# Optimization experiments

Measured on AMD Instinct MI355X. Metric: run time of the kernel, lower is better.

Reference implementation:

```python
import jax, jax.numpy as jnp
import numpy as np

# Tsit5 (Tsitouras 2011) explicit RK tableau coefficients (5th-order solution weights)
A21 = 0.161
A31, A32 = -0.008480655492356989, 0.335480655492357
A41, A42, A43 = 2.8971530571054935, -6.359448489975075, 4.3622954328695815
A51, A52, A53, A54 = 5.325864828439257, -11.748883564062828, 7.4955393428898365, -0.09249506636175525
A61, A62, A63, A64, A65 = 5.86145544294642, -12.92096931784711, 8.159367898576159, -0.071584973281401, -0.028269050394068383
B1, B2, B3, B4, B5, B6 = 0.09646076681806523, 0.01, 0.4798896504144996, 1.379008574103742, -3.290069515436081, 2.324710524099774

BATCH, D, H, T = 4096, 64, 256, 128


def net_apply(y, W1, b1, W2, b2):
    # y: [B, D] -> dy/dt: [B, D]  (MLP vector field, autonomous)
    return jnp.tanh(y @ W1 + b1) @ W2 + b2


def tsit5_step(f, y, h):
    # One explicit Tsit5 step of size h on state y: [B, D]
    k1 = f(y)
    k2 = f(y + h * (A21 * k1))
    k3 = f(y + h * (A31 * k1 + A32 * k2))
    k4 = f(y + h * (A41 * k1 + A42 * k2 + A43 * k3))
    k5 = f(y + h * (A51 * k1 + A52 * k2 + A53 * k3 + A54 * k4))
    k6 = f(y + h * (A61 * k1 + A62 * k2 + A63 * k3 + A64 * k4 + A65 * k5))
    return y + h * (B1 * k1 + B2 * k2 + B3 * k3 + B4 * k4 + B5 * k5 + B6 * k6)


def setup_inputs() -> dict:
    key = jax.random.key(0)
    k0, k1, k2 = jax.random.split(key, 3)
    y0 = jax.random.normal(k0, (BATCH, D), dtype=jnp.float32)
    ts = jnp.arange(T, dtype=jnp.float32) * 0.05  # save times
    W1 = jax.random.normal(k1, (D, H), dtype=jnp.float32) / np.sqrt(D)
    b1 = jnp.zeros((H,), dtype=jnp.float32)
    W2 = jax.random.normal(k2, (H, D), dtype=jnp.float32) / np.sqrt(H)
    b2 = jnp.zeros((D,), dtype=jnp.float32)
    return {"y0": y0, "ts": ts, "W1": W1, "b1": b1, "W2": W2, "b2": b2, "n_sub": 8}


def reference(y0, ts, W1, b1, W2, b2, n_sub):
    # Integrate dy/dt = net(y) with fixed-step Tsit5 (n_sub substeps per save interval),
    # returning the trajectory at save points ts: [B, T, D].
    f = lambda y: net_apply(y, W1, b1, W2, b2)

    def interval(y, dt):
        h = dt / n_sub
        def sub(yc, _):
            return tsit5_step(f, yc, h), None
        y, _ = jax.lax.scan(sub, y, None, length=n_sub)
        return y, y

    dts = jnp.diff(ts)                      # [T-1]
    _, ys = jax.lax.scan(interval, y0, dts)  # [T-1, B, D]
    traj = jnp.concatenate([y0[None], ys], axis=0)  # [T, B, D]
    return jnp.transpose(traj, (1, 0, 2))   # [B, T, D]
```

## Files before the change

### kernel.cpp

```cpp
#include <hip/hip_runtime.h>
#include <hip/hip_bf16.h>

typedef __bf16 bf16x8 __attribute__((ext_vector_type(8)));
typedef float f32x4 __attribute__((ext_vector_type(4)));
typedef unsigned int u32;
typedef u32 u32x4 __attribute__((ext_vector_type(4)));

#define MFMA_B16(a,b,c) __builtin_amdgcn_mfma_f32_16x16x32_bf16((a),(b),(c),0,0,0)

#define A21f 0.161f
#define A31f (-0.008480655492356989f)
#define A32f 0.335480655492357f
#define A41f 2.8971530571054935f
#define A42f (-6.359448489975075f)
#define A43f 4.3622954328695815f
#define A51f 5.325864828439257f
#define A52f (-11.748883564062828f)
#define A53f 7.4955393428898365f
#define A54f (-0.09249506636175525f)
#define A61f 5.86145544294642f
#define A62f (-12.92096931784711f)
#define A63f 8.159367898576159f
#define A64f (-0.071584973281401f)
#define A65f (-0.028269050394068383f)
#define B1f 0.09646076681806523f
#define B2f 0.01f
#define B3f 0.4798896504144996f
#define B4f 1.379008574103742f
#define B5f (-3.290069515436081f)
#define B6f 2.324710524099774f

constexpr int T_SAVE = 128;
constexpr int DIM = 64;
constexpr int HID = 256;

__device__ __forceinline__ float fast_exp2(float x){
#if __has_builtin(__builtin_amdgcn_exp2f)
  return __builtin_amdgcn_exp2f(x);
#else
  return exp2f(x);
#endif
}
__device__ __forceinline__ float fast_rcp(float x){
#if __has_builtin(__builtin_amdgcn_rcpf)
  return __builtin_amdgcn_rcpf(x);
#else
  return 1.0f / x;
#endif
}
__device__ __forceinline__ float tanh_fast(float x){
  float t = fast_exp2(x * 2.8853900817779268f);
  return 1.0f - 2.0f * fast_rcp(t + 1.0f);
}
__device__ __forceinline__ f32x4 splat4(float x){ return f32x4{x,x,x,x}; }

__device__ __forceinline__ u32 pack_hl(float x){
  u32 xu = __float_as_uint(x);
  float lo = x - __uint_as_float(xu & 0xFFFF0000u);
  __bf16 lb = (__bf16)lo;
  unsigned short ls; __builtin_memcpy(&ls, &lb, 2);
  return ((u32)ls << 16) | (xu >> 16);
}
__device__ __forceinline__ void unpack2(const u32* p, bf16x8& ah, bf16x8& al){
  union { u32 d[4]; bf16x8 v; } H, L;
#pragma unroll
  for (int j = 0; j < 4; ++j) {
    H.d[j] = __builtin_amdgcn_perm(p[2*j+1], p[2*j], 0x05040100u);
    L.d[j] = __builtin_amdgcn_perm(p[2*j+1], p[2*j], 0x07060302u);
  }
  ah = H.v; al = L.v;
}

__device__ __forceinline__ int bphys(int row, int kq){
  return kq*16 + (row & 8) + ((row & 7) ^ (kq & 7));
}

__global__ __launch_bounds__(512, 2)
void node_tsit5_kernel(const float* __restrict__ y0, const float* __restrict__ ts,
                       const float* __restrict__ W1g, const float* __restrict__ b1g,
                       const float* __restrict__ W2g, const float* __restrict__ b2g,
                       const int* __restrict__ nsub_p, float* __restrict__ out)
{
  const int tid = (int)threadIdx.x;
  const int w   = tid >> 6;
  const int l   = tid & 63;
  const int c   = l & 15;
  const int g   = l >> 4;
  const bool state = (w < 4);
  const int v   = state ? w : (w - 4);
  const int rowbase = (int)blockIdx.x * 16;

  __shared__ __align__(16) u32 Yp[1024];
  __shared__ __align__(16) u32 Hp[4096];
  __shared__ float ts_s[T_SAVE];

  if (tid < T_SAVE) ts_s[tid] = ts[tid];

  const int nsub = nsub_p[0];

  bf16x8 wf[16];
  float bias[4];
  if (state) {
#pragma unroll
    for (int ks = 0; ks < 8; ++ks)
#pragma unroll
      for (int j = 0; j < 8; ++j) {
        float val = W2g[(ks*32 + g*8 + j)*DIM + (v*16 + c)];
        __bf16 hi = (__bf16)val;
        wf[ks*2    ][j] = hi;
        wf[ks*2 + 1][j] = (__bf16)(val - (float)hi);
      }
    bias[0] = b2g[v*16 + c];
    bias[1] = bias[2] = bias[3] = 0.f;
  } else {
#pragma unroll
    for (int t = 0; t < 4; ++t) {
      const int col = (v*4 + t)*16 + c;
#pragma unroll
      for (int sl = 0; sl < 2; ++sl)
#pragma unroll
        for (int j = 0; j < 8; ++j) {
          float val = W1g[(sl*32 + g*8 + j)*HID + col];
          __bf16 hi = (__bf16)val;
          wf[t*4 + sl*2    ][j] = hi;
          wf[t*4 + sl*2 + 1][j] = (__bf16)(val - (float)hi);
        }
      bias[t] = b1g[col];
    }
  }

  const int rdw0 = bphys(c, 2*g    ) * 4;
  const int rdw1 = bphys(c, 2*g + 1) * 4;
  int yw[4];
#pragma unroll
  for (int s = 0; s < 4; ++s) {
    const int kq = (v & 1)*4 + (c >> 2);
    yw[s] = ((v >> 1)*512) + bphys(4*g + s, kq)*4 + (c & 3);
  }
  int hw[4][4];
  if (!state) {
#pragma unroll
    for (int t = 0; t < 4; ++t) {
      const int T = v*4 + t;
      const int kq = (T & 1)*4 + (c >> 2);
#pragma unroll
      for (int r = 0; r < 4; ++r)
        hw[t][r] = ((T >> 1)*512) + bphys(4*g + r, kq)*4 + (c & 3);
    }
  }

  const int d_ = v*16 + c;
  f32x4 y4 = {0.f,0.f,0.f,0.f};
  if (state) {
#pragma unroll
    for (int s = 0; s < 4; ++s) {
      int row = rowbase + 4*g + s;
      y4[s] = y0[row*DIM + d_];
      out[(size_t)row*(T_SAVE*DIM) + d_] = y4[s];
    }
  }
  __syncthreads();

  f32x4 ysv = y4;

  auto feval = [&]() -> f32x4 {
    if (state) {
#pragma unroll
      for (int s = 0; s < 4; ++s) Yp[yw[s]] = pack_hl(ysv[s]);
    }
    __syncthreads();
    if (!state) {
      u32 py[2][8];
      *(u32x4*)&py[0][0] = *(const u32x4*)&Yp[rdw0];
      *(u32x4*)&py[0][4] = *(const u32x4*)&Yp[rdw1];
      *(u32x4*)&py[1][0] = *(const u32x4*)&Yp[512 + rdw0];
      *(u32x4*)&py[1][4] = *(const u32x4*)&Yp[512 + rdw1];
      bf16x8 ah[2], al[2];
      unpack2(py[0], ah[0], al[0]);
      unpack2(py[1], ah[1], al[1]);
#pragma unroll
      for (int t = 0; t < 4; ++t) {
        f32x4 a0 = {0.f,0.f,0.f,0.f}, a1 = {0.f,0.f,0.f,0.f};
        a0 = MFMA_B16(ah[0], wf[t*4 + 0], a0);
        a1 = MFMA_B16(ah[1], wf[t*4 + 2], a1);
        a0 = MFMA_B16(ah[0], wf[t*4 + 1], a0);
        a1 = MFMA_B16(ah[1], wf[t*4 + 3], a1);
        a0 = MFMA_B16(al[0], wf[t*4 + 0], a0);
        a1 = MFMA_B16(al[1], wf[t*4 + 2], a1);
        f32x4 ht = a0 + a1;
#pragma unroll
        for (int r = 0; r < 4; ++r)
          Hp[hw[t][r]] = pack_hl(tanh_fast(ht[r] + bias[t]));
      }
    }
    __syncthreads();
    f32x4 ret = {0.f,0.f,0.f,0.f};
    if (state) {
      u32 ph[8][8];
#pragma unroll
      for (int ks = 0; ks < 8; ++ks) {
        *(u32x4*)&ph[ks][0] = *(const u32x4*)&Hp[ks*512 + rdw0];
        *(u32x4*)&ph[ks][4] = *(const u32x4*)&Hp[ks*512 + rdw1];
      }
      f32x4 aA = {0.f,0.f,0.f,0.f}, aB = {0.f,0.f,0.f,0.f}, aC = {0.f,0.f,0.f,0.f};
#pragma unroll
      for (int ks = 0; ks < 8; ++ks) {
        bf16x8 ah, al;
        unpack2(ph[ks], ah, al);
        aA = MFMA_B16(ah, wf[ks*2    ], aA);
        aB = MFMA_B16(ah, wf[ks*2 + 1], aB);
        aC = MFMA_B16(al, wf[ks*2    ], aC);
      }
      ret = (aA + aB) + aC + splat4(bias[0]);
    }
    return ret;
  };

  for (int iv = 0; iv < T_SAVE-1; ++iv) {
    const float h = (ts_s[iv+1] - ts_s[iv]) / (float)nsub;
    const f32x4 h4 = splat4(h);
    for (int sub = 0; sub < nsub; ++sub) {
      f32x4 k1 = feval();
      if (state) ysv = y4 + h4 * (splat4(A21f) * k1);
      f32x4 k2 = feval();
      if (state) {
        f32x4 t = splat4(A31f)*k1 + splat4(A32f)*k2;
        ysv = y4 + h4 * t;
      }
      f32x4 k3 = feval();
      if (state) {
        f32x4 t = splat4(A41f)*k1 + splat4(A42f)*k2 + splat4(A43f)*k3;
        ysv = y4 + h4 * t;
      }
      f32x4 k4 = feval();
      if (state) {
        f32x4 t = splat4(A51f)*k1 + splat4(A52f)*k2 + splat4(A53f)*k3
                + splat4(A54f)*k4;
        ysv = y4 + h4 * t;
      }
      f32x4 k5 = feval();
      if (state) {
        f32x4 t = splat4(A61f)*k1 + splat4(A62f)*k2 + splat4(A63f)*k3
                + splat4(A64f)*k4 + splat4(A65f)*k5;
        ysv = y4 + h4 * t;
      }
      f32x4 k6 = feval();
      if (state) {
        f32x4 t = splat4(B1f)*k1 + splat4(B2f)*k2 + splat4(B3f)*k3
                + splat4(B4f)*k4 + splat4(B5f)*k5 + splat4(B6f)*k6;
        y4 = y4 + h4 * t;
        ysv = y4;
      }
    }
    if (state) {
#pragma unroll
      for (int s = 0; s < 4; ++s) {
        int row = rowbase + 4*g + s;
        out[(size_t)row*(T_SAVE*DIM) + (size_t)(iv+1)*DIM + d_] = y4[s];
      }
    }
  }
}

extern "C" void kernel_launch(void* const* d_in, const int* in_sizes, int n_in,
                              void* d_out, int out_size, void* d_ws, size_t ws_size,
                              hipStream_t stream) {
  const float* y0 = (const float*)d_in[0];
  const float* ts = (const float*)d_in[1];
  const float* W1 = (const float*)d_in[2];
  const float* b1 = (const float*)d_in[3];
  const float* W2 = (const float*)d_in[4];
  const float* b2 = (const float*)d_in[5];
  const int* nsub = (const int*)d_in[6];
  float* out = (float*)d_out;

  const int Bnum = in_sizes[0] / DIM;
  const int nblocks = Bnum / 16;
  node_tsit5_kernel<<<nblocks, 512, 0, stream>>>(y0, ts, W1, b1, W2, b2, nsub, out);
}
```

Before: 7.646 ms.

## Replace block barriers with LDS flag-based producer/consumer sync and double buffers

Block-wide __syncthreads between the state and hidden-layer wave groups are replaced with per-wave progress counters in shared memory. Waves spin on these counters with s_sleep, and the Y and H staging buffers are double-buffered. Hidden tiles are interleaved across waves so state waves can start each K-chunk of the second matmul as soon as its two producer tiles are flagged, instead of waiting for the whole hidden layer. The aim is to cut barrier latency on this strictly serial RK chain, at the cost of spin-polling overhead and reliance on LDS ordering via explicit waitcnt.

```diff
diff --git a/kernel.cpp b/kernel.cpp
--- a/kernel.cpp
+++ b/kernel.cpp
@@ -86,177 +86,190 @@
   const int l   = tid & 63;
   const int c   = l & 15;
   const int g   = l >> 4;
-  const bool state = (w < 4);
-  const int v   = state ? w : (w - 4);
+  const bool stateRole = (w >= 4);
+  const int v   = w & 3;
   const int rowbase = (int)blockIdx.x * 16;
 
-  __shared__ __align__(16) u32 Yp[1024];
-  __shared__ __align__(16) u32 Hp[4096];
+  __shared__ __align__(16) u32 Yp[2][1024];
+  __shared__ __align__(16) u32 Hp[2][4096];
+  __shared__ u32 yctr[4];
+  __shared__ u32 hctr[16];
   __shared__ float ts_s[T_SAVE];
 
   if (tid < T_SAVE) ts_s[tid] = ts[tid];
+  if (tid < 16) hctr[tid] = 0;
+  if (tid < 4)  yctr[tid] = 0;
 
   const int nsub = nsub_p[0];
-
-  bf16x8 wf[16];
-  float bias[4];
-  if (state) {
+  const u32 NF = (u32)(T_SAVE - 1) * (u32)nsub * 6u;
+
+  const int rdw0 = bphys(c, 2*g    ) * 4;
+  const int rdw1 = bphys(c, 2*g + 1) * 4;
+
+  __syncthreads();
+
+  if (!stateRole) {
+    bf16x8 wh[4][2], wl[4][2];
+    float b1v[4];
+    int hw_[4][4];
+#pragma unroll
+    for (int t = 0; t < 4; ++t) {
+      const int T = v + 4*t;
+      const int col = T*16 + c;
+#pragma unroll
+      for (int sl = 0; sl < 2; ++sl)
+#pragma unroll
+        for (int j = 0; j < 8; ++j) {
+          float val = W1g[(sl*32 + g*8 + j)*HID + col];
+          __bf16 hi = (__bf16)val;
+          wh[t][sl][j] = hi;
+          wl[t][sl][j] = (__bf16)(val - (float)hi);
+        }
+      b1v[t] = b1g[col];
+      const int kq = (T & 1)*4 + (c >> 2);
+#pragma unroll
+      for (int r = 0; r < 4; ++r)
+        hw_[t][r] = (T >> 1)*512 + bphys(4*g + r, kq)*4 + (c & 3);
+    }
+
+    volatile u32* yc = yctr;
+    for (u32 n = 0; n < NF; ++n) {
+      const u32 need = n + 1u;
+      while (yc[0] < need || yc[1] < need || yc[2] < need || yc[3] < need)
+        __builtin_amdgcn_s_sleep(1);
+      asm volatile("" ::: "memory");
+      const u32* Yb = Yp[n & 1];
+      u32 py[8], pz[8];
+      *(u32x4*)&py[0] = *(const u32x4*)&Yb[rdw0];
+      *(u32x4*)&py[4] = *(const u32x4*)&Yb[rdw1];
+      *(u32x4*)&pz[0] = *(const u32x4*)&Yb[512 + rdw0];
+      *(u32x4*)&pz[4] = *(const u32x4*)&Yb[512 + rdw1];
+      bf16x8 ah0, al0, ah1, al1;
+      unpack2(py, ah0, al0);
+      unpack2(pz, ah1, al1);
+      u32* Hb = Hp[n & 1];
+#pragma unroll
+      for (int t = 0; t < 4; ++t) {
+        f32x4 a0 = {0.f,0.f,0.f,0.f}, a1 = {0.f,0.f,0.f,0.f};
+        a0 = MFMA_B16(ah0, wh[t][0], a0);  a1 = MFMA_B16(ah1, wh[t][1], a1);
+        a0 = MFMA_B16(ah0, wl[t][0], a0);  a1 = MFMA_B16(ah1, wl[t][1], a1);
+        a0 = MFMA_B16(al0, wh[t][0], a0);  a1 = MFMA_B16(al1, wh[t][1], a1);
+        f32x4 ht = a0 + a1;
+#pragma unroll
+        for (int r = 0; r < 4; ++r)
+          Hb[hw_[t][r]] = pack_hl(tanh_fast(ht[r] + b1v[t]));
+        asm volatile("s_waitcnt lgkmcnt(0)" ::: "memory");
+        if (l == 0) *(volatile u32*)&hctr[v + 4*t] = need;
+      }
+    }
+  } else {
+    bf16x8 w2h[8], w2l[8];
 #pragma unroll
     for (int ks = 0; ks < 8; ++ks)
 #pragma unroll
       for (int j = 0; j < 8; ++j) {
         float val = W2g[(ks*32 + g*8 + j)*DIM + (v*16 + c)];
         __bf16 hi = (__bf16)val;
-        wf[ks*2    ][j] = hi;
-        wf[ks*2 + 1][j] = (__bf16)(val - (float)hi);
-      }
-    bias[0] = b2g[v*16 + c];
-    bias[1] = bias[2] = bias[3] = 0.f;
-  } else {
-#pragma unroll
-    for (int t = 0; t < 4; ++t) {
-      const int col = (v*4 + t)*16 + c;
-#pragma unroll
-      for (int sl = 0; sl < 2; ++sl)
-#pragma unroll
-        for (int j = 0; j < 8; ++j) {
-          float val = W1g[(sl*32 + g*8 + j)*HID + col];
-          __bf16 hi = (__bf16)val;
-          wf[t*4 + sl*2    ][j] = hi;
-          wf[t*4 + sl*2 + 1][j] = (__bf16)(val - (float)hi);
-        }
-      bias[t] = b1g[col];
-    }
-  }
-
-  const int rdw0 = bphys(c, 2*g    ) * 4;
-  const int rdw1 = bphys(c, 2*g + 1) * 4;
-  int yw[4];
-#pragma unroll
-  for (int s = 0; s < 4; ++s) {
-    const int kq = (v & 1)*4 + (c >> 2);
-    yw[s] = ((v >> 1)*512) + bphys(4*g + s, kq)*4 + (c & 3);
-  }
-  int hw[4][4];
-  if (!state) {
-#pragma unroll
-    for (int t = 0; t < 4; ++t) {
-      const int T = v*4 + t;
-      const int kq = (T & 1)*4 + (c >> 2);
-#pragma unroll
-      for (int r = 0; r < 4; ++r)
-        hw[t][r] = ((T >> 1)*512) + bphys(4*g + r, kq)*4 + (c & 3);
-    }
-  }
-
-  const int d_ = v*16 + c;
-  f32x4 y4 = {0.f,0.f,0.f,0.f};
-  if (state) {
-#pragma unroll
-    for (int s = 0; s < 4; ++s) {
-      int row = rowbase + 4*g + s;
-      y4[s] = y0[row*DIM + d_];
-      out[(size_t)row*(T_SAVE*DIM) + d_] = y4[s];
-    }
-  }
-  __syncthreads();
-
-  f32x4 ysv = y4;
-
-  auto feval = [&]() -> f32x4 {
-    if (state) {
-#pragma unroll
-      for (int s = 0; s < 4; ++s) Yp[yw[s]] = pack_hl(ysv[s]);
-    }
-    __syncthreads();
-    if (!state) {
-      u32 py[2][8];
-      *(u32x4*)&py[0][0] = *(const u32x4*)&Yp[rdw0];
-      *(u32x4*)&py[0][4] = *(const u32x4*)&Yp[rdw1];
-      *(u32x4*)&py[1][0] = *(const u32x4*)&Yp[512 + rdw0];
-      *(u32x4*)&py[1][4] = *(const u32x4*)&Yp[512 + rdw1];
-      bf16x8 ah[2], al[2];
-      unpack2(py[0], ah[0], al[0]);
-      unpack2(py[1], ah[1], al[1]);
-#pragma unroll
-      for (int t = 0; t < 4; ++t) {
-        f32x4 a0 = {0.f,0.f,0.f,0.f}, a1 = {0.f,0.f,0.f,0.f};
-        a0 = MFMA_B16(ah[0], wf[t*4 + 0], a0);
-        a1 = MFMA_B16(ah[1], wf[t*4 + 2], a1);
-        a0 = MFMA_B16(ah[0], wf[t*4 + 1], a0);
-        a1 = MFMA_B16(ah[1], wf[t*4 + 3], a1);
-        a0 = MFMA_B16(al[0], wf[t*4 + 0], a0);
-        a1 = MFMA_B16(al[1], wf[t*4 + 2], a1);
-        f32x4 ht = a0 + a1;
-#pragma unroll
-        for (int r = 0; r < 4; ++r)
-          Hp[hw[t][r]] = pack_hl(tanh_fast(ht[r] + bias[t]));
-      }
-    }
-    __syncthreads();
-    f32x4 ret = {0.f,0.f,0.f,0.f};
-    if (state) {
-      u32 ph[8][8];
+        w2h[ks][j] = hi;
+        w2l[ks][j] = (__bf16)(val - (float)hi);
+      }
+    const float b2v = b2g[v*16 + c];
+    const int d_ = v*16 + c;
+
+    int yw[4];
+#pragma unroll
+    for (int s4 = 0; s4 < 4; ++s4) {
+      const int kq = (v & 1)*4 + (c >> 2);
+      yw[s4] = (v >> 1)*512 + bphys(4*g + s4, kq)*4 + (c & 3);
+    }
+
+    f32x4 y4;
+#pragma unroll
+    for (int s4 = 0; s4 < 4; ++s4) {
+      int row = rowbase + 4*g + s4;
+      y4[s4] = y0[row*DIM + d_];
+      out[(size_t)row*(T_SAVE*DIM) + d_] = y4[s4];
+    }
+
+    auto stage = [&](const f32x4& val, u32 n){
+      u32* Yb = Yp[n & 1];
+#pragma unroll
+      for (int s4 = 0; s4 < 4; ++s4) Yb[yw[s4]] = pack_hl(val[s4]);
+      asm volatile("s_waitcnt lgkmcnt(0)" ::: "memory");
+      if (l == 0) *(volatile u32*)&yctr[v] = n + 1u;
+    };
+
+    auto consume = [&](u32 n) -> f32x4 {
+      const u32* Hb = Hp[n & 1];
+      const u32 need = n + 1u;
+      f32x4 aA = {0.f,0.f,0.f,0.f}, aB = {0.f,0.f,0.f,0.f}, aC = {0.f,0.f,0.f,0.f};
 #pragma unroll
       for (int ks = 0; ks < 8; ++ks) {
-        *(u32x4*)&ph[ks][0] = *(const u32x4*)&Hp[ks*512 + rdw0];
-        *(u32x4*)&ph[ks][4] = *(const u32x4*)&Hp[ks*512 + rdw1];
-      }
-      f32x4 aA = {0.f,0.f,0.f,0.f}, aB = {0.f,0.f,0.f,0.f}, aC = {0.f,0.f,0.f,0.f};
-#pragma unroll
-      for (int ks = 0; ks < 8; ++ks) {
+        volatile u32* hc = &hctr[2*ks];
+        while (hc[0] < need || hc[1] < need) __builtin_amdgcn_s_sleep(1);
+        asm volatile("" ::: "memory");
+        u32 ph[8];
+        *(u32x4*)&ph[0] = *(const u32x4*)&Hb[ks*512 + rdw0];
+        *(u32x4*)&ph[4] = *(const u32x4*)&Hb[ks*512 + rdw1];
         bf16x8 ah, al;
-        unpack2(ph[ks], ah, al);
-        aA = MFMA_B16(ah, wf[ks*2    ], aA);
-        aB = MFMA_B16(ah, wf[ks*2 + 1], aB);
-        aC = MFMA_B16(al, wf[ks*2    ], aC);
-      }
-      ret = (aA + aB) + aC + splat4(bias[0]);
-    }
-    return ret;
-  };
-
-  for (int iv = 0; iv < T_SAVE-1; ++iv) {
-    const float h = (ts_s[iv+1] - ts_s[iv]) / (float)nsub;
-    const f32x4 h4 = splat4(h);
-    for (int sub = 0; sub < nsub; ++sub) {
-      f32x4 k1 = feval();
-      if (state) ysv = y4 + h4 * (splat4(A21f) * k1);
-      f32x4 k2 = feval();
-      if (state) {
-        f32x4 t = splat4(A31f)*k1 + splat4(A32f)*k2;
-        ysv = y4 + h4 * t;
-      }
-      f32x4 k3 = feval();
-      if (state) {
-        f32x4 t = splat4(A41f)*k1 + splat4(A42f)*k2 + splat4(A43f)*k3;
-        ysv = y4 + h4 * t;
-      }
-      f32x4 k4 = feval();
-      if (state) {
-        f32x4 t = splat4(A51f)*k1 + splat4(A52f)*k2 + splat4(A53f)*k3
-                + splat4(A54f)*k4;
-        ysv = y4 + h4 * t;
-      }
-      f32x4 k5 = feval();
-      if (state) {
-        f32x4 t = splat4(A61f)*k1 + splat4(A62f)*k2 + splat4(A63f)*k3
-                + splat4(A64f)*k4 + splat4(A65f)*k5;
-        ysv = y4 + h4 * t;
-      }
-      f32x4 k6 = feval();
-      if (state) {
-        f32x4 t = splat4(B1f)*k1 + splat4(B2f)*k2 + splat4(B3f)*k3
-                + splat4(B4f)*k4 + splat4(B5f)*k5 + splat4(B6f)*k6;
-        y4 = y4 + h4 * t;
-        ysv = y4;
-      }
-    }
-    if (state) {
-#pragma unroll
-      for (int s = 0; s < 4; ++s) {
-        int row = rowbase + 4*g + s;
-        out[(size_t)row*(T_SAVE*DIM) + (size_t)(iv+1)*DIM + d_] = y4[s];
+        unpack2(ph, ah, al);
+        aA = MFMA_B16(ah, w2h[ks], aA);
+        aB = MFMA_B16(ah, w2l[ks], aB);
+        aC = MFMA_B16(al, w2h[ks], aC);
+      }
+      return (aA + aB) + aC + splat4(b2v);
+    };
+
+    f32x4 ysv = y4;
+    stage(ysv, 0);
+    u32 ep = 0;
+
+    for (int iv = 0; iv < T_SAVE-1; ++iv) {
+      const float h = (ts_s[iv+1] - ts_s[iv]) / (float)nsub;
+      const f32x4 h4 = splat4(h);
+      for (int sub = 0; sub < nsub; ++sub) {
+        f32x4 k1 = consume(ep);
+        ysv = y4 + h4 * (splat4(A21f) * k1);
+        stage(ysv, ep+1); ++ep;
+        f32x4 k2 = consume(ep);
+        {
+          f32x4 t = splat4(A31f)*k1 + splat4(A32f)*k2;
+          ysv = y4 + h4 * t;
+        }
+        stage(ysv, ep+1); ++ep;
+        f32x4 k3 = consume(ep);
+        {
+          f32x4 t = splat4(A41f)*k1 + splat4(A42f)*k2 + splat4(A43f)*k3;
+          ysv = y4 + h4 * t;
+        }
+        stage(ysv, ep+1); ++ep;
+        f32x4 k4 = consume(ep);
+        {
+          f32x4 t = splat4(A51f)*k1 + splat4(A52f)*k2 + splat4(A53f)*k3
+                  + splat4(A54f)*k4;
+          ysv = y4 + h4 * t;
+        }
+        stage(ysv, ep+1); ++ep;
+        f32x4 k5 = consume(ep);
+        {
+          f32x4 t = splat4(A61f)*k1 + splat4(A62f)*k2 + splat4(A63f)*k3
+                  + splat4(A64f)*k4 + splat4(A65f)*k5;
+          ysv = y4 + h4 * t;
+        }
+        stage(ysv, ep+1); ++ep;
+        f32x4 k6 = consume(ep);
+        {
+          f32x4 t = splat4(B1f)*k1 + splat4(B2f)*k2 + splat4(B3f)*k3
+                  + splat4(B4f)*k4 + splat4(B5f)*k5 + splat4(B6f)*k6;
+          y4 = y4 + h4 * t;
+          ysv = y4;
+        }
+        stage(ysv, ep+1); ++ep;
+      }
+#pragma unroll
+      for (int s4 = 0; s4 < 4; ++s4) {
+        int row = rowbase + 4*g + s4;
+        out[(size_t)row*(T_SAVE*DIM) + (size_t)(iv+1)*DIM + d_] = y4[s4];
       }
     }
   }
```

Result: slower. 13.45 ms (+76.0%).
